# Kernel tuning notes

Hardware: AMD Instinct MI355X
Metric: run time of the kernel (lower is better)

The kernel has to match this reference:

```python
import jax, jax.numpy as jnp
import numpy as np

N_EMBD = 1024
QK_DIM = 16


def setup_inputs() -> dict:
    key = jax.random.key(0)
    k1, k2, k3, k4, k5 = jax.random.split(key, 5)
    b, s = 8, 2048
    lim = 1.0 / np.sqrt(N_EMBD)  # torch Linear default init range
    return {
        "x": jax.random.normal(k1, (b, s, N_EMBD), dtype=jnp.float32),
        "w_q": jax.random.uniform(k2, (QK_DIM, N_EMBD), minval=-lim, maxval=lim, dtype=jnp.float32),
        "b_q": jax.random.uniform(k3, (QK_DIM,), minval=-lim, maxval=lim, dtype=jnp.float32),
        "w_k": jax.random.uniform(k4, (QK_DIM, N_EMBD), minval=-lim, maxval=lim, dtype=jnp.float32),
        "b_k": jax.random.uniform(k5, (QK_DIM,), minval=-lim, maxval=lim, dtype=jnp.float32),
    }


def reference(x, w_q, b_q, w_k, b_k):
    # x: [b, s, d_model]
    s = x.shape[-2]
    q = jnp.einsum("bsd,ed->bse", x, w_q) + b_q  # [b, s, qk_dim]
    k = jnp.einsum("bsd,ed->bse", x, w_k) + b_k  # [b, s, qk_dim]
    scale = 1.0 / jnp.sqrt(jnp.asarray(QK_DIM, dtype=x.dtype))
    mask = jnp.arange(s)[:, None] >= jnp.arange(s)[None, :]  # causal [s, s]
    scores = jnp.einsum("bqe,bke->bqk", q, k) * scale  # [b, s, s]
    scores = jnp.where(mask[None], scores, jnp.asarray(-10000.0, dtype=x.dtype))
    probs = jax.nn.softmax(scores, axis=-1)
    return jnp.einsum("bqk,bkv->bqv", probs, x)  # identity OV: weighted sum of x
```

## Files before the change

kernel.cpp:

```cpp
#include <hip/hip_runtime.h>

typedef __attribute__((ext_vector_type(4))) float  f32x4;
typedef __attribute__((ext_vector_type(8))) short  bf16x8;
typedef __attribute__((ext_vector_type(4))) unsigned int u32x4;

#define MFMA16(a,b,c) __builtin_amdgcn_mfma_f32_16x16x32_bf16(a,b,c,0,0,0)
#define SCL   0.360673760f
#define PBIAS 17.3123405f

static __device__ __forceinline__ unsigned short f2bf(float f){
  unsigned int u = __float_as_uint(f);
  u += 0x7fffu + ((u>>16)&1u);
  return (unsigned short)(u>>16);
}
static __device__ __forceinline__ unsigned int pk2(float a, float b){
  return (unsigned)f2bf(a) | (((unsigned)f2bf(b))<<16);
}
static __device__ __forceinline__ float expfast(float a){
  float e; asm("v_exp_f32 %0, %1" : "=v"(e) : "v"(a)); return e;
}

__global__ __launch_bounds__(256,2) void prep_kernel(
    const float* __restrict__ x,  const float* __restrict__ wq, const float* __restrict__ bq,
    const float* __restrict__ wk, const float* __restrict__ bk,
    unsigned short* __restrict__ qws, unsigned short* __restrict__ kws,
    unsigned char* __restrict__ xpk)
{
  __shared__ __align__(16) unsigned short wlds[32*1032];
  __shared__ __align__(16) unsigned short xlds[64*72];
  const int t  = threadIdx.x;
  const int r0 = blockIdx.x<<6;
  const int b  = r0>>11;
  const int s0 = r0&2047;
  const int l = t&63, w = t>>6, g = l>>4, li = l&15;

  { const int n = t>>3, part = t&7;
    const float* wsrc = (n<16) ? (wq + n*1024) : (wk + (n-16)*1024);
    #pragma unroll
    for(int cc=0; cc<16; ++cc){
      const int d = part*128 + cc*8;
      f32x4 f0 = *(const f32x4*)(wsrc + d);
      f32x4 f1 = *(const f32x4*)(wsrc + d + 4);
      u32x4 p;
      p[0]=pk2(f0[0],f0[1]); p[1]=pk2(f0[2],f0[3]);
      p[2]=pk2(f1[0],f1[1]); p[3]=pk2(f1[2],f1[3]);
      *(u32x4*)(&wlds[n*1032 + d]) = p;
    }
  }
  __syncthreads();

  f32x4 acc0 = {0.f,0.f,0.f,0.f};
  f32x4 acc1 = {0.f,0.f,0.f,0.f};
  const int srow = t>>2, dch = t&3;
  const int dd = t&63, sch = t>>6;

  unsigned char* pdst = xpk + ((size_t)(b*64 + (s0>>5) + (sch>>1)))*65536
                      + (size_t)(dd>>4)*1024 + (size_t)(sch&1)*512 + (size_t)(dd&15)*16;

  for(int it=0; it<16; ++it){
    { const float* xp = x + (size_t)(r0+srow)*1024 + it*64 + dch*16;
      f32x4 a0 = *(const f32x4*)(xp);
      f32x4 a1 = *(const f32x4*)(xp+4);
      f32x4 a2 = *(const f32x4*)(xp+8);
      f32x4 a3 = *(const f32x4*)(xp+12);
      u32x4 p0, p1;
      p0[0]=pk2(a0[0],a0[1]); p0[1]=pk2(a0[2],a0[3]);
      p0[2]=pk2(a1[0],a1[1]); p0[3]=pk2(a1[2],a1[3]);
      p1[0]=pk2(a2[0],a2[1]); p1[1]=pk2(a2[2],a2[3]);
      p1[2]=pk2(a3[0],a3[1]); p1[3]=pk2(a3[2],a3[3]);
      *(u32x4*)(&xlds[srow*72 + dch*16])     = p0;
      *(u32x4*)(&xlds[srow*72 + dch*16 + 8]) = p1;
    }
    __syncthreads();
    #pragma unroll
    for(int ks=0; ks<2; ++ks){
      bf16x8 a  = *(const bf16x8*)(&xlds[(16*w+li)*72       + ks*32 + g*8]);
      bf16x8 b0 = *(const bf16x8*)(&wlds[ li*1032     + it*64 + ks*32 + g*8]);
      bf16x8 b1 = *(const bf16x8*)(&wlds[(16+li)*1032 + it*64 + ks*32 + g*8]);
      acc0 = MFMA16(a,b0,acc0);
      acc1 = MFMA16(a,b1,acc1);
    }
    {
      unsigned short v[16];
      #pragma unroll
      for(int jj=0; jj<16; ++jj) v[jj] = xlds[(sch*16 + jj)*72 + dd];
      u32x4 o0, o1;
      o0[0]=(unsigned)v[0]|((unsigned)v[1]<<16);   o0[1]=(unsigned)v[2]|((unsigned)v[3]<<16);
      o0[2]=(unsigned)v[4]|((unsigned)v[5]<<16);   o0[3]=(unsigned)v[6]|((unsigned)v[7]<<16);
      o1[0]=(unsigned)v[8]|((unsigned)v[9]<<16);   o1[1]=(unsigned)v[10]|((unsigned)v[11]<<16);
      o1[2]=(unsigned)v[12]|((unsigned)v[13]<<16); o1[3]=(unsigned)v[14]|((unsigned)v[15]<<16);
      unsigned char* dst = pdst + (size_t)it*4096;
      *(u32x4*)(dst)       = o0;
      *(u32x4*)(dst + 256) = o1;
    }
    __syncthreads();
  }
  #pragma unroll
  for(int reg=0; reg<4; ++reg){
    const int sr = r0 + 16*w + 4*g + reg;
    qws[(size_t)sr*16 + li] = f2bf(acc0[reg] + bq[li]);
    kws[(size_t)sr*16 + li] = f2bf(acc1[reg] + bk[li]);
  }
}

__global__ __launch_bounds__(256,3) void attn_kernel(
    const unsigned short* __restrict__ qws, const unsigned short* __restrict__ kws,
    const unsigned char* __restrict__ xpk, float* __restrict__ out)
{
  __shared__ __align__(16) unsigned char pshare[16384];
  __shared__ float psL[64];
  const int t = threadIdx.x;
  const int l = t&63, w = t>>6, g = l>>4, li = l&15;
  const int bi = blockIdx.x;
  const int b = bi&7;
  const int j = bi>>3;
  const int qb = 31-(j>>2), dq = j&3;
  const int q0 = qb<<6, d0 = dq<<8, nt = qb + 1;

  const int kperm = ((li>>2)<<3) + (li&3);

  const bf16x8 zero8 = {0,0,0,0,0,0,0,0};
  bf16x8 qfr = zero8;
  if(g < 2) qfr = *(const bf16x8*)(qws + ((size_t)(b*2048 + q0 + 16*w + li)<<4) + 8*g);
  const int qg = q0 + 16*w + li;

  f32x4 acc[4][4];
  #pragma unroll
  for(int i=0;i<4;++i)
    #pragma unroll
    for(int jj=0;jj<4;++jj){ acc[i][jj][0]=0.f; acc[i][jj][1]=0.f; acc[i][jj][2]=0.f; acc[i][jj][3]=0.f; }
  float sp = 0.f;

  const unsigned char* xq = xpk + (size_t)(b*64)*65536 + (size_t)(16*dq + 4*w)*1024 + l*16;
  const unsigned short* kp0 = kws + ((size_t)(b*2048 + kperm)<<4) + 8*g;

  bf16x8 k1 = *(const bf16x8*)(kp0);
  bf16x8 k2 = *(const bf16x8*)(kp0 + 64);
  bf16x8 k3 = *(const bf16x8*)(kp0 + 512);
  bf16x8 k4 = *(const bf16x8*)(kp0 + 576);

  int buf = 0;
  for(int tt=0; tt<nt; ++tt){
    const int kv0 = tt<<6;
    u32x4 xc[4], xd[4];
    const unsigned char* xqt = xq + (size_t)(tt*2)*65536;
    #pragma unroll
    for(int df=0; df<4; ++df){
      xc[df] = *(const u32x4*)(xqt + df*1024);
      xd[df] = *(const u32x4*)(xqt + 65536 + df*1024);
    }
    f32x4 z = {0.f,0.f,0.f,0.f};
    f32x4 s1 = MFMA16(k1, qfr, z);
    f32x4 s2 = MFMA16(k2, qfr, z);
    f32x4 s3 = MFMA16(k3, qfr, z);
    f32x4 s4 = MFMA16(k4, qfr, z);
    const int tn = (tt+1 < nt) ? tt+1 : tt;
    const unsigned short* kpn = kp0 + (size_t)(tn<<6)*16;
    bf16x8 n1 = *(const bf16x8*)(kpn);
    bf16x8 n2 = *(const bf16x8*)(kpn + 64);
    bf16x8 n3 = *(const bf16x8*)(kpn + 512);
    bf16x8 n4 = *(const bf16x8*)(kpn + 576);
    float p[16];
    if(tt < nt-1){
      #pragma unroll
      for(int r=0;r<4;++r){
        p[r]    = expfast(fmaf(s1[r], SCL, -PBIAS));
        p[4+r]  = expfast(fmaf(s2[r], SCL, -PBIAS));
        p[8+r]  = expfast(fmaf(s3[r], SCL, -PBIAS));
        p[12+r] = expfast(fmaf(s4[r], SCL, -PBIAS));
      }
    } else {
      const int b1 = kv0 + 8*g, b2 = kv0 + 32 + 8*g;
      #pragma unroll
      for(int r=0;r<4;++r){
        p[r]    = (b1+r   <= qg) ? expfast(fmaf(s1[r], SCL, -PBIAS)) : 0.f;
        p[4+r]  = (b1+4+r <= qg) ? expfast(fmaf(s2[r], SCL, -PBIAS)) : 0.f;
        p[8+r]  = (b2+r   <= qg) ? expfast(fmaf(s3[r], SCL, -PBIAS)) : 0.f;
        p[12+r] = (b2+4+r <= qg) ? expfast(fmaf(s4[r], SCL, -PBIAS)) : 0.f;
      }
    }
    sp += (((p[0]+p[1])+(p[2]+p[3])) + ((p[4]+p[5])+(p[6]+p[7])))
        + (((p[8]+p[9])+(p[10]+p[11])) + ((p[12]+p[13])+(p[14]+p[15])));
    { u32x4 avA, avB;
      asm("v_cvt_pk_bf16_f32 %0, %1, %2" : "=v"(avA[0]) : "v"(p[0]),  "v"(p[1]));
      asm("v_cvt_pk_bf16_f32 %0, %1, %2" : "=v"(avA[1]) : "v"(p[2]),  "v"(p[3]));
      asm("v_cvt_pk_bf16_f32 %0, %1, %2" : "=v"(avA[2]) : "v"(p[4]),  "v"(p[5]));
      asm("v_cvt_pk_bf16_f32 %0, %1, %2" : "=v"(avA[3]) : "v"(p[6]),  "v"(p[7]));
      asm("v_cvt_pk_bf16_f32 %0, %1, %2" : "=v"(avB[0]) : "v"(p[8]),  "v"(p[9]));
      asm("v_cvt_pk_bf16_f32 %0, %1, %2" : "=v"(avB[1]) : "v"(p[10]), "v"(p[11]));
      asm("v_cvt_pk_bf16_f32 %0, %1, %2" : "=v"(avB[2]) : "v"(p[12]), "v"(p[13]));
      asm("v_cvt_pk_bf16_f32 %0, %1, %2" : "=v"(avB[3]) : "v"(p[14]), "v"(p[15]));
      *(u32x4*)(&pshare[buf*8192 + w*2048 +        l*16]) = avA;
      *(u32x4*)(&pshare[buf*8192 + w*2048 + 1024 + l*16]) = avB;
    }
    asm volatile("s_waitcnt lgkmcnt(0)" ::: "memory");
    __builtin_amdgcn_sched_barrier(0);
    __builtin_amdgcn_s_barrier();
    __builtin_amdgcn_sched_barrier(0);
    __builtin_amdgcn_s_setprio(1);
    #pragma unroll
    for(int qf=0; qf<4; ++qf){
      bf16x8 aA = *(const bf16x8*)(&pshare[buf*8192 + qf*2048 +        l*16]);
      bf16x8 aB = *(const bf16x8*)(&pshare[buf*8192 + qf*2048 + 1024 + l*16]);
      #pragma unroll
      for(int df=0; df<4; ++df){
        acc[qf][df] = MFMA16(aA, *(const bf16x8*)(&xc[df]), acc[qf][df]);
        acc[qf][df] = MFMA16(aB, *(const bf16x8*)(&xd[df]), acc[qf][df]);
      }
    }
    __builtin_amdgcn_s_setprio(0);
    buf ^= 1; k1=n1; k2=n2; k3=n3; k4=n4;
  }

  float r_ = sp;
  r_ += __shfl_xor(r_, 16);
  r_ += __shfl_xor(r_, 32);
  if(l < 16) psL[16*w + l] = r_;
  __syncthreads();
  #pragma unroll
  for(int qf=0; qf<4; ++qf){
    const f32x4 pv = *(const f32x4*)(&psL[16*qf + 4*g]);
    #pragma unroll
    for(int reg=0; reg<4; ++reg){
      const float inv = 1.0f/pv[reg];
      float* op = out + (size_t)(b*2048 + q0 + 16*qf + 4*g + reg)*1024 + d0 + 64*w + li;
      #pragma unroll
      for(int df=0; df<4; ++df) op[df*16] = acc[qf][df][reg]*inv;
    }
  }
}

extern "C" void kernel_launch(void* const* d_in, const int* in_sizes, int n_in,
                              void* d_out, int out_size, void* d_ws, size_t ws_size,
                              hipStream_t stream) {
  (void)in_sizes; (void)n_in; (void)out_size; (void)ws_size;
  const float* x  = (const float*)d_in[0];
  const float* wq = (const float*)d_in[1];
  const float* bq = (const float*)d_in[2];
  const float* wk = (const float*)d_in[3];
  const float* bk = (const float*)d_in[4];
  float* out = (float*)d_out;
  char* ws = (char*)d_ws;
  unsigned short* qws = (unsigned short*)(ws);
  unsigned short* kws = (unsigned short*)(ws + (512<<10));
  unsigned char*  xpk = (unsigned char*)(ws + (2<<20));
  hipLaunchKernelGGL(prep_kernel, dim3(256), dim3(256), 0, stream, x, wq, bq, wk, bk, qws, kws, xpk);
  hipLaunchKernelGGL(attn_kernel, dim3(1024), dim3(256), 0, stream, qws, kws, xpk, out);
}
```

Baseline: 68.79 us.

## Software-pipeline PV MFMA one tile behind QK/exp to overlap with softmax

Restructures the main loop so that each iteration computes scores and exponentials for tile tt while running the P·X MFMAs for tile tt-1 from the other pshare buffer. The barrier now only guards the P write and read handoff. A tail block after the loop finishes the last tile. This aims to overlap the exp and LDS-write phase with matrix work and to hide X global-load latency, at the cost of more live registers and a double-buffer dependency.

```diff
diff --git a/kernel.cpp b/kernel.cpp
--- a/kernel.cpp
+++ b/kernel.cpp
@@ -142,13 +142,6 @@
   int buf = 0;
   for(int tt=0; tt<nt; ++tt){
     const int kv0 = tt<<6;
-    u32x4 xc[4], xd[4];
-    const unsigned char* xqt = xq + (size_t)(tt*2)*65536;
-    #pragma unroll
-    for(int df=0; df<4; ++df){
-      xc[df] = *(const u32x4*)(xqt + df*1024);
-      xd[df] = *(const u32x4*)(xqt + 65536 + df*1024);
-    }
     f32x4 z = {0.f,0.f,0.f,0.f};
     f32x4 s1 = MFMA16(k1, qfr, z);
     f32x4 s2 = MFMA16(k2, qfr, z);
@@ -160,6 +153,15 @@
     bf16x8 n2 = *(const bf16x8*)(kpn + 64);
     bf16x8 n3 = *(const bf16x8*)(kpn + 512);
     bf16x8 n4 = *(const bf16x8*)(kpn + 576);
+    u32x4 xc[4], xd[4];
+    if(tt > 0){
+      const unsigned char* xqt = xq + (size_t)((tt-1)*2)*65536;
+      #pragma unroll
+      for(int df=0; df<4; ++df){
+        xc[df] = *(const u32x4*)(xqt + df*1024);
+        xd[df] = *(const u32x4*)(xqt + 65536 + df*1024);
+      }
+    }
     float p[16];
     if(tt < nt-1){
       #pragma unroll
@@ -193,23 +195,46 @@
       *(u32x4*)(&pshare[buf*8192 + w*2048 +        l*16]) = avA;
       *(u32x4*)(&pshare[buf*8192 + w*2048 + 1024 + l*16]) = avB;
     }
+    if(tt > 0){
+      __builtin_amdgcn_s_setprio(1);
+      const int pb = (buf^1)*8192;
+      #pragma unroll
+      for(int qf=0; qf<4; ++qf){
+        bf16x8 aA = *(const bf16x8*)(&pshare[pb + qf*2048 +        l*16]);
+        bf16x8 aB = *(const bf16x8*)(&pshare[pb + qf*2048 + 1024 + l*16]);
+        #pragma unroll
+        for(int df=0; df<4; ++df){
+          acc[qf][df] = MFMA16(aA, *(const bf16x8*)(&xc[df]), acc[qf][df]);
+          acc[qf][df] = MFMA16(aB, *(const bf16x8*)(&xd[df]), acc[qf][df]);
+        }
+      }
+      __builtin_amdgcn_s_setprio(0);
+    }
     asm volatile("s_waitcnt lgkmcnt(0)" ::: "memory");
     __builtin_amdgcn_sched_barrier(0);
     __builtin_amdgcn_s_barrier();
     __builtin_amdgcn_sched_barrier(0);
-    __builtin_amdgcn_s_setprio(1);
+    buf ^= 1; k1=n1; k2=n2; k3=n3; k4=n4;
+  }
+  {
+    u32x4 xc[4], xd[4];
+    const unsigned char* xqt = xq + (size_t)((nt-1)*2)*65536;
+    #pragma unroll
+    for(int df=0; df<4; ++df){
+      xc[df] = *(const u32x4*)(xqt + df*1024);
+      xd[df] = *(const u32x4*)(xqt + 65536 + df*1024);
+    }
+    const int pb = (buf^1)*8192;
     #pragma unroll
     for(int qf=0; qf<4; ++qf){
-      bf16x8 aA = *(const bf16x8*)(&pshare[buf*8192 + qf*2048 +        l*16]);
-      bf16x8 aB = *(const bf16x8*)(&pshare[buf*8192 + qf*2048 + 1024 + l*16]);
+      bf16x8 aA = *(const bf16x8*)(&pshare[pb + qf*2048 +        l*16]);
+      bf16x8 aB = *(const bf16x8*)(&pshare[pb + qf*2048 + 1024 + l*16]);
       #pragma unroll
       for(int df=0; df<4; ++df){
         acc[qf][df] = MFMA16(aA, *(const bf16x8*)(&xc[df]), acc[qf][df]);
         acc[qf][df] = MFMA16(aB, *(const bf16x8*)(&xd[df]), acc[qf][df]);
       }
     }
-    __builtin_amdgcn_s_setprio(0);
-    buf ^= 1; k1=n1; k2=n2; k3=n3; k4=n4;
   }
 
   float r_ = sp;
```

New measurement: 69.15 us. About the same (+0.5%).

## Pair long and short causal query blocks per workgroup for load balance

Applied to the files above, without the earlier changes.

Each workgroup now handles two query blocks, qb=31-pid and qb=pid, in sequence, so every workgroup does the same total number of KV tiles (33). The grid shrinks from 1024 to 512 blocks. This removes the causal triangle's load imbalance and the long tail from heavy blocks. In exchange each block runs longer with one less wave of parallel blocks, and an extra barrier is added before psL is reused.

```diff
diff --git a/kernel.cpp b/kernel.cpp
--- a/kernel.cpp
+++ b/kernel.cpp
@@ -113,119 +113,126 @@
   const int l = t&63, w = t>>6, g = l>>4, li = l&15;
   const int bi = blockIdx.x;
   const int b = bi&7;
-  const int j = bi>>3;
-  const int qb = 31-(j>>2), dq = j&3;
-  const int q0 = qb<<6, d0 = dq<<8, nt = qb + 1;
+  const int r = bi>>3;
+  const int dq = r&3, pid = r>>2;
+  const int d0 = dq<<8;
 
   const int kperm = ((li>>2)<<3) + (li&3);
 
   const bf16x8 zero8 = {0,0,0,0,0,0,0,0};
-  bf16x8 qfr = zero8;
-  if(g < 2) qfr = *(const bf16x8*)(qws + ((size_t)(b*2048 + q0 + 16*w + li)<<4) + 8*g);
-  const int qg = q0 + 16*w + li;
-
-  f32x4 acc[4][4];
-  #pragma unroll
-  for(int i=0;i<4;++i)
-    #pragma unroll
-    for(int jj=0;jj<4;++jj){ acc[i][jj][0]=0.f; acc[i][jj][1]=0.f; acc[i][jj][2]=0.f; acc[i][jj][3]=0.f; }
-  float sp = 0.f;
-
   const unsigned char* xq = xpk + (size_t)(b*64)*65536 + (size_t)(16*dq + 4*w)*1024 + l*16;
   const unsigned short* kp0 = kws + ((size_t)(b*2048 + kperm)<<4) + 8*g;
 
-  bf16x8 k1 = *(const bf16x8*)(kp0);
-  bf16x8 k2 = *(const bf16x8*)(kp0 + 64);
-  bf16x8 k3 = *(const bf16x8*)(kp0 + 512);
-  bf16x8 k4 = *(const bf16x8*)(kp0 + 576);
-
   int buf = 0;
-  for(int tt=0; tt<nt; ++tt){
-    const int kv0 = tt<<6;
-    u32x4 xc[4], xd[4];
-    const unsigned char* xqt = xq + (size_t)(tt*2)*65536;
-    #pragma unroll
-    for(int df=0; df<4; ++df){
-      xc[df] = *(const u32x4*)(xqt + df*1024);
-      xd[df] = *(const u32x4*)(xqt + 65536 + df*1024);
-    }
-    f32x4 z = {0.f,0.f,0.f,0.f};
-    f32x4 s1 = MFMA16(k1, qfr, z);
-    f32x4 s2 = MFMA16(k2, qfr, z);
-    f32x4 s3 = MFMA16(k3, qfr, z);
-    f32x4 s4 = MFMA16(k4, qfr, z);
-    const int tn = (tt+1 < nt) ? tt+1 : tt;
-    const unsigned short* kpn = kp0 + (size_t)(tn<<6)*16;
-    bf16x8 n1 = *(const bf16x8*)(kpn);
-    bf16x8 n2 = *(const bf16x8*)(kpn + 64);
-    bf16x8 n3 = *(const bf16x8*)(kpn + 512);
-    bf16x8 n4 = *(const bf16x8*)(kpn + 576);
-    float p[16];
-    if(tt < nt-1){
-      #pragma unroll
-      for(int r=0;r<4;++r){
-        p[r]    = expfast(fmaf(s1[r], SCL, -PBIAS));
-        p[4+r]  = expfast(fmaf(s2[r], SCL, -PBIAS));
-        p[8+r]  = expfast(fmaf(s3[r], SCL, -PBIAS));
-        p[12+r] = expfast(fmaf(s4[r], SCL, -PBIAS));
-      }
-    } else {
-      const int b1 = kv0 + 8*g, b2 = kv0 + 32 + 8*g;
-      #pragma unroll
-      for(int r=0;r<4;++r){
-        p[r]    = (b1+r   <= qg) ? expfast(fmaf(s1[r], SCL, -PBIAS)) : 0.f;
-        p[4+r]  = (b1+4+r <= qg) ? expfast(fmaf(s2[r], SCL, -PBIAS)) : 0.f;
-        p[8+r]  = (b2+r   <= qg) ? expfast(fmaf(s3[r], SCL, -PBIAS)) : 0.f;
-        p[12+r] = (b2+4+r <= qg) ? expfast(fmaf(s4[r], SCL, -PBIAS)) : 0.f;
-      }
-    }
-    sp += (((p[0]+p[1])+(p[2]+p[3])) + ((p[4]+p[5])+(p[6]+p[7])))
-        + (((p[8]+p[9])+(p[10]+p[11])) + ((p[12]+p[13])+(p[14]+p[15])));
-    { u32x4 avA, avB;
-      asm("v_cvt_pk_bf16_f32 %0, %1, %2" : "=v"(avA[0]) : "v"(p[0]),  "v"(p[1]));
-      asm("v_cvt_pk_bf16_f32 %0, %1, %2" : "=v"(avA[1]) : "v"(p[2]),  "v"(p[3]));
-      asm("v_cvt_pk_bf16_f32 %0, %1, %2" : "=v"(avA[2]) : "v"(p[4]),  "v"(p[5]));
-      asm("v_cvt_pk_bf16_f32 %0, %1, %2" : "=v"(avA[3]) : "v"(p[6]),  "v"(p[7]));
-      asm("v_cvt_pk_bf16_f32 %0, %1, %2" : "=v"(avB[0]) : "v"(p[8]),  "v"(p[9]));
-      asm("v_cvt_pk_bf16_f32 %0, %1, %2" : "=v"(avB[1]) : "v"(p[10]), "v"(p[11]));
-      asm("v_cvt_pk_bf16_f32 %0, %1, %2" : "=v"(avB[2]) : "v"(p[12]), "v"(p[13]));
-      asm("v_cvt_pk_bf16_f32 %0, %1, %2" : "=v"(avB[3]) : "v"(p[14]), "v"(p[15]));
-      *(u32x4*)(&pshare[buf*8192 + w*2048 +        l*16]) = avA;
-      *(u32x4*)(&pshare[buf*8192 + w*2048 + 1024 + l*16]) = avB;
-    }
-    asm volatile("s_waitcnt lgkmcnt(0)" ::: "memory");
-    __builtin_amdgcn_sched_barrier(0);
-    __builtin_amdgcn_s_barrier();
-    __builtin_amdgcn_sched_barrier(0);
-    __builtin_amdgcn_s_setprio(1);
+  #pragma unroll 1
+  for(int seg=0; seg<2; ++seg){
+    const int qb = (seg==0) ? 31-pid : pid;
+    const int q0 = qb<<6, nt = qb + 1;
+
+    bf16x8 qfr = zero8;
+    if(g < 2) qfr = *(const bf16x8*)(qws + ((size_t)(b*2048 + q0 + 16*w + li)<<4) + 8*g);
+    const int qg = q0 + 16*w + li;
+
+    f32x4 acc[4][4];
+    #pragma unroll
+    for(int i=0;i<4;++i)
+      #pragma unroll
+      for(int jj=0;jj<4;++jj){ acc[i][jj][0]=0.f; acc[i][jj][1]=0.f; acc[i][jj][2]=0.f; acc[i][jj][3]=0.f; }
+    float sp = 0.f;
+
+    bf16x8 k1 = *(const bf16x8*)(kp0);
+    bf16x8 k2 = *(const bf16x8*)(kp0 + 64);
+    bf16x8 k3 = *(const bf16x8*)(kp0 + 512);
+    bf16x8 k4 = *(const bf16x8*)(kp0 + 576);
+
+    for(int tt=0; tt<nt; ++tt){
+      const int kv0 = tt<<6;
+      u32x4 xc[4], xd[4];
+      const unsigned char* xqt = xq + (size_t)(tt*2)*65536;
+      #pragma unroll
+      for(int df=0; df<4; ++df){
+        xc[df] = *(const u32x4*)(xqt + df*1024);
+        xd[df] = *(const u32x4*)(xqt + 65536 + df*1024);
+      }
+      f32x4 z = {0.f,0.f,0.f,0.f};
+      f32x4 s1 = MFMA16(k1, qfr, z);
+      f32x4 s2 = MFMA16(k2, qfr, z);
+      f32x4 s3 = MFMA16(k3, qfr, z);
+      f32x4 s4 = MFMA16(k4, qfr, z);
+      const int tn = (tt+1 < nt) ? tt+1 : tt;
+      const unsigned short* kpn = kp0 + (size_t)(tn<<6)*16;
+      bf16x8 n1 = *(const bf16x8*)(kpn);
+      bf16x8 n2 = *(const bf16x8*)(kpn + 64);
+      bf16x8 n3 = *(const bf16x8*)(kpn + 512);
+      bf16x8 n4 = *(const bf16x8*)(kpn + 576);
+      float p[16];
+      if(tt < nt-1){
+        #pragma unroll
+        for(int rr=0;rr<4;++rr){
+          p[rr]    = expfast(fmaf(s1[rr], SCL, -PBIAS));
+          p[4+rr]  = expfast(fmaf(s2[rr], SCL, -PBIAS));
+          p[8+rr]  = expfast(fmaf(s3[rr], SCL, -PBIAS));
+          p[12+rr] = expfast(fmaf(s4[rr], SCL, -PBIAS));
+        }
+      } else {
+        const int b1 = kv0 + 8*g, b2 = kv0 + 32 + 8*g;
+        #pragma unroll
+        for(int rr=0;rr<4;++rr){
+          p[rr]    = (b1+rr   <= qg) ? expfast(fmaf(s1[rr], SCL, -PBIAS)) : 0.f;
+          p[4+rr]  = (b1+4+rr <= qg) ? expfast(fmaf(s2[rr], SCL, -PBIAS)) : 0.f;
+          p[8+rr]  = (b2+rr   <= qg) ? expfast(fmaf(s3[rr], SCL, -PBIAS)) : 0.f;
+          p[12+rr] = (b2+4+rr <= qg) ? expfast(fmaf(s4[rr], SCL, -PBIAS)) : 0.f;
+        }
+      }
+      sp += (((p[0]+p[1])+(p[2]+p[3])) + ((p[4]+p[5])+(p[6]+p[7])))
+          + (((p[8]+p[9])+(p[10]+p[11])) + ((p[12]+p[13])+(p[14]+p[15])));
+      { u32x4 avA, avB;
+        asm("v_cvt_pk_bf16_f32 %0, %1, %2" : "=v"(avA[0]) : "v"(p[0]),  "v"(p[1]));
+        asm("v_cvt_pk_bf16_f32 %0, %1, %2" : "=v"(avA[1]) : "v"(p[2]),  "v"(p[3]));
+        asm("v_cvt_pk_bf16_f32 %0, %1, %2" : "=v"(avA[2]) : "v"(p[4]),  "v"(p[5]));
+        asm("v_cvt_pk_bf16_f32 %0, %1, %2" : "=v"(avA[3]) : "v"(p[6]),  "v"(p[7]));
+        asm("v_cvt_pk_bf16_f32 %0, %1, %2" : "=v"(avB[0]) : "v"(p[8]),  "v"(p[9]));
+        asm("v_cvt_pk_bf16_f32 %0, %1, %2" : "=v"(avB[1]) : "v"(p[10]), "v"(p[11]));
+        asm("v_cvt_pk_bf16_f32 %0, %1, %2" : "=v"(avB[2]) : "v"(p[12]), "v"(p[13]));
+        asm("v_cvt_pk_bf16_f32 %0, %1, %2" : "=v"(avB[3]) : "v"(p[14]), "v"(p[15]));
+        *(u32x4*)(&pshare[buf*8192 + w*2048 +        l*16]) = avA;
+        *(u32x4*)(&pshare[buf*8192 + w*2048 + 1024 + l*16]) = avB;
+      }
+      asm volatile("s_waitcnt lgkmcnt(0)" ::: "memory");
+      __builtin_amdgcn_sched_barrier(0);
+      __builtin_amdgcn_s_barrier();
+      __builtin_amdgcn_sched_barrier(0);
+      __builtin_amdgcn_s_setprio(1);
+      #pragma unroll
+      for(int qf=0; qf<4; ++qf){
+        bf16x8 aA = *(const bf16x8*)(&pshare[buf*8192 + qf*2048 +        l*16]);
+        bf16x8 aB = *(const bf16x8*)(&pshare[buf*8192 + qf*2048 + 1024 + l*16]);
+        #pragma unroll
+        for(int df=0; df<4; ++df){
+          acc[qf][df] = MFMA16(aA, *(const bf16x8*)(&xc[df]), acc[qf][df]);
+          acc[qf][df] = MFMA16(aB, *(const bf16x8*)(&xd[df]), acc[qf][df]);
+        }
+      }
+      __builtin_amdgcn_s_setprio(0);
+      buf ^= 1; k1=n1; k2=n2; k3=n3; k4=n4;
+    }
+
+    float r_ = sp;
+    r_ += __shfl_xor(r_, 16);
+    r_ += __shfl_xor(r_, 32);
+    __syncthreads();
+    if(l < 16) psL[16*w + l] = r_;
+    __syncthreads();
     #pragma unroll
     for(int qf=0; qf<4; ++qf){
-      bf16x8 aA = *(const bf16x8*)(&pshare[buf*8192 + qf*2048 +        l*16]);
-      bf16x8 aB = *(const bf16x8*)(&pshare[buf*8192 + qf*2048 + 1024 + l*16]);
-      #pragma unroll
-      for(int df=0; df<4; ++df){
-        acc[qf][df] = MFMA16(aA, *(const bf16x8*)(&xc[df]), acc[qf][df]);
-        acc[qf][df] = MFMA16(aB, *(const bf16x8*)(&xd[df]), acc[qf][df]);
-      }
-    }
-    __builtin_amdgcn_s_setprio(0);
-    buf ^= 1; k1=n1; k2=n2; k3=n3; k4=n4;
-  }
-
-  float r_ = sp;
-  r_ += __shfl_xor(r_, 16);
-  r_ += __shfl_xor(r_, 32);
-  if(l < 16) psL[16*w + l] = r_;
-  __syncthreads();
-  #pragma unroll
-  for(int qf=0; qf<4; ++qf){
-    const f32x4 pv = *(const f32x4*)(&psL[16*qf + 4*g]);
-    #pragma unroll
-    for(int reg=0; reg<4; ++reg){
-      const float inv = 1.0f/pv[reg];
-      float* op = out + (size_t)(b*2048 + q0 + 16*qf + 4*g + reg)*1024 + d0 + 64*w + li;
-      #pragma unroll
-      for(int df=0; df<4; ++df) op[df*16] = acc[qf][df][reg]*inv;
+      const f32x4 pv = *(const f32x4*)(&psL[16*qf + 4*g]);
+      #pragma unroll
+      for(int reg=0; reg<4; ++reg){
+        const float inv = 1.0f/pv[reg];
+        float* op = out + (size_t)(b*2048 + q0 + 16*qf + 4*g + reg)*1024 + d0 + 64*w + li;
+        #pragma unroll
+        for(int df=0; df<4; ++df) op[df*16] = acc[qf][df][reg]*inv;
+      }
     }
   }
 }
@@ -245,5 +252,5 @@
   unsigned short* kws = (unsigned short*)(ws + (512<<10));
   unsigned char*  xpk = (unsigned char*)(ws + (2<<20));
   hipLaunchKernelGGL(prep_kernel, dim3(256), dim3(256), 0, stream, x, wq, bq, wk, bk, qws, kws, xpk);
-  hipLaunchKernelGGL(attn_kernel, dim3(1024), dim3(256), 0, stream, qws, kws, xpk, out);
-}
+  hipLaunchKernelGGL(attn_kernel, dim3(512), dim3(256), 0, stream, qws, kws, xpk, out);
+}
```

Result: slower. 70.24 us (+2.1%).
